# Kernel tuning notes

Measured on AMD Instinct MI355X. Metric: run time of the kernel, lower is better.

The kernel has to match this reference:

```python
import jax, jax.numpy as jnp
import numpy as np

N_NODES = 100000
N_EDGES = 3200000
D_IN = 128
D_OUT = 128


def setup_inputs() -> dict:
    key = jax.random.key(0)
    k1, k2, k3, k4, k5 = jax.random.split(key, 5)
    x = jax.random.normal(k1, (N_NODES, D_IN), dtype=jnp.float32)
    edge_row = jnp.sort(jax.random.randint(k2, (N_EDGES,), 0, N_NODES))
    edge_col = jax.random.randint(k3, (N_EDGES,), 0, N_NODES)
    edge_val = jax.random.uniform(k4, (N_EDGES,), dtype=jnp.float32)
    W = jax.random.normal(k5, (D_IN, D_OUT), dtype=jnp.float32) * (1.0 / np.sqrt(D_IN))
    return {"x": x, "edge_row": edge_row, "edge_col": edge_col,
            "edge_val": edge_val, "W": W}


def reference(x, edge_row, edge_col, edge_val, W):
    # h = spmm(adj_norm, x): gather source features, scale by edge weight,
    # scatter-add into destination rows.
    msgs = edge_val[:, None] * x[edge_col]            # [E, D_IN]
    h = jax.ops.segment_sum(msgs, edge_row, num_segments=N_NODES)  # [N, D_IN]
    # dense linear projection (no bias)
    return h @ W                                       # [N, D_OUT]
```

## Files before the change

kernel.cpp:

```cpp
#include <hip/hip_runtime.h>
#include <hip/hip_bf16.h>

#define D 128
#define D2U 64

typedef __attribute__((ext_vector_type(8))) short  short8;
typedef __attribute__((ext_vector_type(4))) float  f32x4;
typedef __attribute__((ext_vector_type(2))) float  f32x2;

__device__ __forceinline__ unsigned f2bf(float f) {
    unsigned u = __float_as_uint(f);
    u += 0x7FFFu + ((u >> 16) & 1u);
    return u >> 16;
}
__device__ __forceinline__ unsigned pk2(float a, float b) {
    return f2bf(a) | (f2bf(b) << 16);
}
__device__ __forceinline__ float bflo(unsigned u) { return __uint_as_float(u << 16); }
__device__ __forceinline__ float bfhi(unsigned u) { return __uint_as_float(u & 0xFFFF0000u); }

__global__ __launch_bounds__(256, 2) void gemm_mfma_kernel(
    const float* __restrict__ x, const float* __restrict__ W,
    unsigned* __restrict__ y, int n_nodes, int ntiles)
{
    __shared__ unsigned short Wt[D * D];

    const int t = threadIdx.x;

    {
        const float4* W4 = reinterpret_cast<const float4*>(W);
#pragma unroll
        for (int m = 0; m < 16; ++m) {
            const int idx4 = m * 256 + t;
            const int k  = idx4 >> 5;
            const int c0 = (idx4 & 31) << 2;
            const float4 w = W4[idx4];
            const float wv[4] = {w.x, w.y, w.z, w.w};
#pragma unroll
            for (int i = 0; i < 4; ++i) {
                const int c    = c0 + i;
                const int slot = (k >> 3) ^ (c & 15);
                Wt[c * 128 + slot * 8 + (k & 7)] = (unsigned short)f2bf(wv[i]);
            }
        }
    }
    __syncthreads();

    const int lane = t & 63;
    const int cl   = lane & 15;
    const int g    = lane >> 4;

    short8 wf[8][4];
#pragma unroll
    for (int ct = 0; ct < 8; ++ct)
#pragma unroll
        for (int ks = 0; ks < 4; ++ks) {
            const int c    = ct * 16 + cl;
            const int slot = (ks * 4 + g) ^ cl;
            wf[ct][ks] = *reinterpret_cast<const short8*>(&Wt[c * 128 + slot * 8]);
        }

    const int wave   = (blockIdx.x << 2) | (t >> 6);
    const int nwaves = gridDim.x << 2;

#define LOADX(rt_, buf_)                                                      \
    {                                                                         \
        int r_ = (rt_) * 16 + cl;                                             \
        if (r_ >= n_nodes) r_ = n_nodes - 1;                                  \
        const float* p_ = x + (size_t)r_ * D + g * 8;                         \
        _Pragma("unroll")                                                     \
        for (int ks_ = 0; ks_ < 4; ++ks_) {                                   \
            buf_[2 * ks_]     = *reinterpret_cast<const float4*>(p_ + ks_ * 32);     \
            buf_[2 * ks_ + 1] = *reinterpret_cast<const float4*>(p_ + ks_ * 32 + 4); \
        }                                                                     \
    }

#define COMPUTE(rt_, buf_)                                                    \
    {                                                                         \
        f32x4 acc_[8];                                                        \
        _Pragma("unroll")                                                     \
        for (int ct_ = 0; ct_ < 8; ++ct_) acc_[ct_] = (f32x4)(0.f);           \
        _Pragma("unroll")                                                     \
        for (int ks_ = 0; ks_ < 4; ++ks_) {                                   \
            short8 xf_;                                                       \
            unsigned* xu_ = reinterpret_cast<unsigned*>(&xf_);                \
            const float4 a_ = buf_[2 * ks_], b_ = buf_[2 * ks_ + 1];          \
            xu_[0] = pk2(a_.x, a_.y); xu_[1] = pk2(a_.z, a_.w);               \
            xu_[2] = pk2(b_.x, b_.y); xu_[3] = pk2(b_.z, b_.w);               \
            _Pragma("unroll")                                                 \
            for (int ct_ = 0; ct_ < 8; ++ct_)                                 \
                acc_[ct_] = __builtin_amdgcn_mfma_f32_16x16x32_bf16(          \
                    wf[ct_][ks_], xf_, acc_[ct_], 0, 0, 0);                   \
        }                                                                     \
        const int r_ = (rt_) * 16 + cl;                                       \
        if (r_ < n_nodes) {                                                   \
            unsigned* yp_ = y + (size_t)r_ * D2U + g * 2;                     \
            _Pragma("unroll")                                                 \
            for (int ct_ = 0; ct_ < 8; ++ct_) {                               \
                uint2 v2_ = make_uint2(pk2(acc_[ct_][0], acc_[ct_][1]),       \
                                       pk2(acc_[ct_][2], acc_[ct_][3]));      \
                *reinterpret_cast<uint2*>(yp_ + ct_ * 8) = v2_;               \
            }                                                                 \
        }                                                                     \
    }

    int rt = wave;
    if (rt >= ntiles) return;
    float4 bufA[8], bufB[8];
    LOADX(rt, bufA);
    while (true) {
        int nxt = rt + nwaves;
        if (nxt < ntiles) {
            LOADX(nxt, bufB);
            COMPUTE(rt, bufA);
            rt = nxt;
            nxt = rt + nwaves;
            if (nxt < ntiles) {
                LOADX(nxt, bufA);
                COMPUTE(rt, bufB);
                rt = nxt;
            } else { COMPUTE(rt, bufB); break; }
        } else { COMPUTE(rt, bufA); break; }
    }
#undef LOADX
#undef COMPUTE
}

__global__ __launch_bounds__(256) void build_rowptr_kernel(
    const int* __restrict__ row, int* __restrict__ ptr, int n_edges, int n_nodes)
{
    int e = blockIdx.x * blockDim.x + threadIdx.x;
    if (e > n_edges) return;
    int lo, hi;
    if (e == 0)            { lo = -1;               hi = row[0];   }
    else if (e == n_edges) { lo = row[n_edges - 1]; hi = n_nodes;  }
    else {
        lo = row[e - 1];
        hi = row[e];
        if (lo == hi) return;
    }
    for (int r = lo + 1; r <= hi; ++r) ptr[r] = e;
}

__global__ __launch_bounds__(256) void spmm_kernel(
    const uint4* __restrict__ yb4, const int* __restrict__ ptr,
    const int* __restrict__ col, const float* __restrict__ val,
    float4* __restrict__ out4, int n_nodes, int n_edges)
{
    const int gid  = blockIdx.x * blockDim.x + threadIdx.x;
    const int w    = gid >> 6;
    const int lane = threadIdx.x & 63;
    const int q    = lane >> 4;
    const int ql   = lane & 15;
    const int row  = (w << 2) + q;
    const bool valid = (row < n_nodes);

    int s = 0, e = 0;
    if (valid) { s = ptr[row]; e = ptr[row + 1]; }

    const int base = s & ~3;
    const int nb   = valid ? ((e - base + 3) >> 2) : 0;

    f32x2 a0 = {0.f, 0.f}, a1 = {0.f, 0.f}, a2 = {0.f, 0.f}, a3 = {0.f, 0.f};

    int4   C0, C1;
    float4 V0, V1;
    uint4  U[4], T[4];

#define CVLOAD(b_, C_, V_)                                                   \
    {                                                                        \
        const int o_ = base + ((b_) << 2);                                   \
        if (o_ + 4 <= n_edges) {                                             \
            C_ = *reinterpret_cast<const int4*>(col + o_);                   \
            V_ = *reinterpret_cast<const float4*>(val + o_);                 \
        } else {                                                             \
            const int m_ = n_edges - 1;                                      \
            C_.x = col[min(o_ + 0, m_)]; C_.y = col[min(o_ + 1, m_)];        \
            C_.z = col[min(o_ + 2, m_)]; C_.w = col[min(o_ + 3, m_)];        \
            V_.x = val[min(o_ + 0, m_)]; V_.y = val[min(o_ + 1, m_)];        \
            V_.z = val[min(o_ + 2, m_)]; V_.w = val[min(o_ + 3, m_)];        \
        }                                                                    \
        V_.x = (o_ + 0 >= s && o_ + 0 < e) ? V_.x : 0.f;                     \
        V_.y = (o_ + 1 >= s && o_ + 1 < e) ? V_.y : 0.f;                     \
        V_.z = (o_ + 2 >= s && o_ + 2 < e) ? V_.z : 0.f;                     \
        V_.w = (o_ + 3 >= s && o_ + 3 < e) ? V_.w : 0.f;                     \
    }

#define GATHER(C_, U_)                                                       \
    {                                                                        \
        U_[0] = yb4[(size_t)C_.x * 16 + ql];                                 \
        U_[1] = yb4[(size_t)C_.y * 16 + ql];                                 \
        U_[2] = yb4[(size_t)C_.z * 16 + ql];                                 \
        U_[3] = yb4[(size_t)C_.w * 16 + ql];                                 \
    }

#define CONSUME1(u_, v_)                                                     \
    {                                                                        \
        f32x2 vv_; vv_.x = (v_); vv_.y = (v_);                               \
        f32x2 t_;                                                            \
        t_.x = bflo(u_.x); t_.y = bfhi(u_.x); a0 += vv_ * t_;                \
        t_.x = bflo(u_.y); t_.y = bfhi(u_.y); a1 += vv_ * t_;                \
        t_.x = bflo(u_.z); t_.y = bfhi(u_.z); a2 += vv_ * t_;                \
        t_.x = bflo(u_.w); t_.y = bfhi(u_.w); a3 += vv_ * t_;                \
    }
#define CONSUME(U_, V_)                                                      \
    {                                                                        \
        CONSUME1(U_[0], V_.x); CONSUME1(U_[1], V_.y);                        \
        CONSUME1(U_[2], V_.z); CONSUME1(U_[3], V_.w);                        \
    }

#define ITER(b_, Ca_, Va_, Cb_, Vb_, Ua_, Ub_)                               \
    {                                                                        \
        if ((b_) + 1 < nb) GATHER(Cb_, Ub_);                                 \
        CONSUME(Ua_, Va_);                                                   \
        if ((b_) + 2 < nb) CVLOAD((b_) + 2, Ca_, Va_);                       \
    }

    if (nb > 0) {
        CVLOAD(0, C0, V0);
        GATHER(C0, U);
        if (nb > 1) CVLOAD(1, C1, V1);

        int b = 0;
        while (true) {
            ITER(b, C0, V0, C1, V1, U, T);
            if (++b >= nb) break;
            ITER(b, C1, V1, C0, V0, T, U);
            if (++b >= nb) break;
        }
    }
#undef CVLOAD
#undef GATHER
#undef CONSUME1
#undef CONSUME
#undef ITER

    if (valid) {
        f32x4 o1, o2;
        o1.x = a0.x; o1.y = a0.y; o1.z = a1.x; o1.w = a1.y;
        o2.x = a2.x; o2.y = a2.y; o2.z = a3.x; o2.w = a3.y;
        f32x4* op = reinterpret_cast<f32x4*>(out4 + (size_t)row * 32 + (ql << 1));
        __builtin_nontemporal_store(o1, op);
        __builtin_nontemporal_store(o2, op + 1);
    }
}

extern "C" void kernel_launch(void* const* d_in, const int* in_sizes, int n_in,
                              void* d_out, int out_size, void* d_ws, size_t ws_size,
                              hipStream_t stream)
{
    const float* x        = (const float*)d_in[0];
    const int*   edge_row = (const int*)  d_in[1];
    const int*   edge_col = (const int*)  d_in[2];
    const float* edge_val = (const float*)d_in[3];
    const float* W        = (const float*)d_in[4];
    float*       out      = (float*)d_out;

    const int n_nodes = in_sizes[0] / D;
    const int n_edges = in_sizes[1];
    const int ntiles  = (n_nodes + 15) / 16;

    unsigned* y   = (unsigned*)d_ws;
    int*      ptr = (int*)((char*)d_ws + (size_t)n_nodes * D2U * sizeof(unsigned));

    gemm_mfma_kernel<<<512, 256, 0, stream>>>(x, W, y, n_nodes, ntiles);

    {
        int blocks = (n_edges + 1 + 255) / 256;
        build_rowptr_kernel<<<blocks, 256, 0, stream>>>(edge_row, ptr, n_edges, n_nodes);
    }
    {
        int nwaves = (n_nodes + 3) / 4;
        int blocks = (nwaves + 3) / 4;
        spmm_kernel<<<blocks, 256, 0, stream>>>((const uint4*)y, ptr,
                                                edge_col, edge_val,
                                                (float4*)out, n_nodes, n_edges);
    }
}
```

Measured before the change: 156.9 us.

## Slice projected features by column and pin slices to XCDs for L2 locality

```diff
diff --git a/kernel.cpp b/kernel.cpp
--- a/kernel.cpp
+++ b/kernel.cpp
@@ -2,7 +2,7 @@
 #include <hip/hip_bf16.h>
 
 #define D 128
-#define D2U 64
+#define NSLICE 8
 
 typedef __attribute__((ext_vector_type(8))) short  short8;
 typedef __attribute__((ext_vector_type(4))) float  f32x4;
@@ -26,6 +26,7 @@
     __shared__ unsigned short Wt[D * D];
 
     const int t = threadIdx.x;
+    const size_t NN = (size_t)n_nodes;
 
     {
         const float4* W4 = reinterpret_cast<const float4*>(W);
@@ -94,12 +95,12 @@
         }                                                                     \
         const int r_ = (rt_) * 16 + cl;                                       \
         if (r_ < n_nodes) {                                                   \
-            unsigned* yp_ = y + (size_t)r_ * D2U + g * 2;                     \
             _Pragma("unroll")                                                 \
             for (int ct_ = 0; ct_ < 8; ++ct_) {                               \
                 uint2 v2_ = make_uint2(pk2(acc_[ct_][0], acc_[ct_][1]),       \
                                        pk2(acc_[ct_][2], acc_[ct_][3]));      \
-                *reinterpret_cast<uint2*>(yp_ + ct_ * 8) = v2_;               \
+                unsigned* yp_ = y + ((size_t)ct_ * NN + r_) * 8 + g * 2;      \
+                *reinterpret_cast<uint2*>(yp_) = v2_;                         \
             }                                                                 \
         }                                                                     \
     }
@@ -142,30 +143,27 @@
     for (int r = lo + 1; r <= hi; ++r) ptr[r] = e;
 }
 
-__global__ __launch_bounds__(256) void spmm_kernel(
-    const uint4* __restrict__ yb4, const int* __restrict__ ptr,
+__global__ void zero_queue_kernel(int* __restrict__ q) {
+    if (threadIdx.x < NSLICE) q[threadIdx.x] = 0;
+}
+
+__global__ __launch_bounds__(256, 8) void spmm_sliced_kernel(
+    const unsigned* __restrict__ ys,
+    const int* __restrict__ ptr,
     const int* __restrict__ col, const float* __restrict__ val,
-    float4* __restrict__ out4, int n_nodes, int n_edges)
-{
-    const int gid  = blockIdx.x * blockDim.x + threadIdx.x;
-    const int w    = gid >> 6;
+    float* __restrict__ out, int* __restrict__ queue,
+    int n_nodes, int n_edges, int rblocks)
+{
+    unsigned xcd;
+    asm volatile("s_getreg_b32 %0, hwreg(HW_REG_XCC_ID)" : "=s"(xcd));
+    xcd &= (NSLICE - 1);
+
+    const int w    = threadIdx.x >> 6;
     const int lane = threadIdx.x & 63;
-    const int q    = lane >> 4;
-    const int ql   = lane & 15;
-    const int row  = (w << 2) + q;
-    const bool valid = (row < n_nodes);
-
-    int s = 0, e = 0;
-    if (valid) { s = ptr[row]; e = ptr[row + 1]; }
-
-    const int base = s & ~3;
-    const int nb   = valid ? ((e - base + 3) >> 2) : 0;
-
-    f32x2 a0 = {0.f, 0.f}, a1 = {0.f, 0.f}, a2 = {0.f, 0.f}, a3 = {0.f, 0.f};
-
-    int4   C0, C1;
-    float4 V0, V1;
-    uint4  U[4], T[4];
+    const int rl   = lane >> 3;
+    const int d    = lane & 7;
+
+    __shared__ int s_idx;
 
 #define CVLOAD(b_, C_, V_)                                                   \
     {                                                                        \
@@ -185,64 +183,74 @@
         V_.z = (o_ + 2 >= s && o_ + 2 < e) ? V_.z : 0.f;                     \
         V_.w = (o_ + 3 >= s && o_ + 3 < e) ? V_.w : 0.f;                     \
     }
-
 #define GATHER(C_, U_)                                                       \
     {                                                                        \
-        U_[0] = yb4[(size_t)C_.x * 16 + ql];                                 \
-        U_[1] = yb4[(size_t)C_.y * 16 + ql];                                 \
-        U_[2] = yb4[(size_t)C_.z * 16 + ql];                                 \
-        U_[3] = yb4[(size_t)C_.w * 16 + ql];                                 \
-    }
-
-#define CONSUME1(u_, v_)                                                     \
-    {                                                                        \
-        f32x2 vv_; vv_.x = (v_); vv_.y = (v_);                               \
-        f32x2 t_;                                                            \
-        t_.x = bflo(u_.x); t_.y = bfhi(u_.x); a0 += vv_ * t_;                \
-        t_.x = bflo(u_.y); t_.y = bfhi(u_.y); a1 += vv_ * t_;                \
-        t_.x = bflo(u_.z); t_.y = bfhi(u_.z); a2 += vv_ * t_;                \
-        t_.x = bflo(u_.w); t_.y = bfhi(u_.w); a3 += vv_ * t_;                \
+        U_[0] = ybase[(size_t)C_.x << 3];                                    \
+        U_[1] = ybase[(size_t)C_.y << 3];                                    \
+        U_[2] = ybase[(size_t)C_.z << 3];                                    \
+        U_[3] = ybase[(size_t)C_.w << 3];                                    \
     }
 #define CONSUME(U_, V_)                                                      \
     {                                                                        \
-        CONSUME1(U_[0], V_.x); CONSUME1(U_[1], V_.y);                        \
-        CONSUME1(U_[2], V_.z); CONSUME1(U_[3], V_.w);                        \
-    }
-
-#define ITER(b_, Ca_, Va_, Cb_, Vb_, Ua_, Ub_)                               \
-    {                                                                        \
-        if ((b_) + 1 < nb) GATHER(Cb_, Ub_);                                 \
-        CONSUME(Ua_, Va_);                                                   \
-        if ((b_) + 2 < nb) CVLOAD((b_) + 2, Ca_, Va_);                       \
-    }
-
-    if (nb > 0) {
-        CVLOAD(0, C0, V0);
-        GATHER(C0, U);
-        if (nb > 1) CVLOAD(1, C1, V1);
-
-        int b = 0;
-        while (true) {
-            ITER(b, C0, V0, C1, V1, U, T);
-            if (++b >= nb) break;
-            ITER(b, C1, V1, C0, V0, T, U);
-            if (++b >= nb) break;
+        f32x2 t_, vv_;                                                       \
+        t_.x = bflo(U_[0]); t_.y = bfhi(U_[0]);                              \
+        vv_.x = V_.x; vv_.y = V_.x; acc += vv_ * t_;                         \
+        t_.x = bflo(U_[1]); t_.y = bfhi(U_[1]);                              \
+        vv_.x = V_.y; vv_.y = V_.y; acc += vv_ * t_;                         \
+        t_.x = bflo(U_[2]); t_.y = bfhi(U_[2]);                              \
+        vv_.x = V_.z; vv_.y = V_.z; acc += vv_ * t_;                         \
+        t_.x = bflo(U_[3]); t_.y = bfhi(U_[3]);                              \
+        vv_.x = V_.w; vv_.y = V_.w; acc += vv_ * t_;                         \
+    }
+
+    for (int sl = 0; sl < NSLICE; ++sl) {
+        const int slice = (xcd + sl) & (NSLICE - 1);
+        const unsigned* ybase = ys + (size_t)slice * n_nodes * 8 + d;
+
+        for (;;) {
+            if (threadIdx.x == 0) s_idx = atomicAdd(queue + slice, 1);
+            __syncthreads();
+            const int rblk = s_idx;
+            __syncthreads();
+            if (rblk >= rblocks) break;
+
+            const int row = (rblk << 5) + (w << 3) + rl;
+            if (row < n_nodes) {
+                const int s = ptr[row];
+                const int e = ptr[row + 1];
+                const int base = s & ~3;
+                const int nb = (e - base + 3) >> 2;
+
+                f32x2 acc; acc.x = 0.f; acc.y = 0.f;
+                int4   C0, C1;
+                float4 V0, V1;
+                unsigned U[4], T[4];
+
+                if (nb > 0) {
+                    CVLOAD(0, C0, V0);
+                    GATHER(C0, U);
+                    if (nb > 1) CVLOAD(1, C1, V1);
+                    int b = 0;
+                    while (true) {
+                        if (b + 1 < nb) GATHER(C1, T);
+                        CONSUME(U, V0);
+                        if (b + 2 < nb) CVLOAD(b + 2, C0, V0);
+                        if (++b >= nb) break;
+                        if (b + 1 < nb) GATHER(C0, U);
+                        CONSUME(T, V1);
+                        if (b + 2 < nb) CVLOAD(b + 2, C1, V1);
+                        if (++b >= nb) break;
+                    }
+                }
+
+                float* op = out + (size_t)row * D + slice * 16 + d * 2;
+                __builtin_nontemporal_store(acc, reinterpret_cast<f32x2*>(op));
+            }
         }
     }
 #undef CVLOAD
 #undef GATHER
-#undef CONSUME1
 #undef CONSUME
-#undef ITER
-
-    if (valid) {
-        f32x4 o1, o2;
-        o1.x = a0.x; o1.y = a0.y; o1.z = a1.x; o1.w = a1.y;
-        o2.x = a2.x; o2.y = a2.y; o2.z = a3.x; o2.w = a3.y;
-        f32x4* op = reinterpret_cast<f32x4*>(out4 + (size_t)row * 32 + (ql << 1));
-        __builtin_nontemporal_store(o1, op);
-        __builtin_nontemporal_store(o2, op + 1);
-    }
 }
 
 extern "C" void kernel_launch(void* const* d_in, const int* in_sizes, int n_in,
@@ -259,9 +267,13 @@
     const int n_nodes = in_sizes[0] / D;
     const int n_edges = in_sizes[1];
     const int ntiles  = (n_nodes + 15) / 16;
-
-    unsigned* y   = (unsigned*)d_ws;
-    int*      ptr = (int*)((char*)d_ws + (size_t)n_nodes * D2U * sizeof(unsigned));
+    const int rblocks = (n_nodes + 31) / 32;
+
+    unsigned* y     = (unsigned*)d_ws;
+    int*      ptr   = (int*)((char*)d_ws + (size_t)n_nodes * 256);
+    int*      queue = ptr + (n_nodes + 1);
+
+    zero_queue_kernel<<<1, 64, 0, stream>>>(queue);
 
     gemm_mfma_kernel<<<512, 256, 0, stream>>>(x, W, y, n_nodes, ntiles);
 
@@ -269,11 +281,8 @@
         int blocks = (n_edges + 1 + 255) / 256;
         build_rowptr_kernel<<<blocks, 256, 0, stream>>>(edge_row, ptr, n_edges, n_nodes);
     }
-    {
-        int nwaves = (n_nodes + 3) / 4;
-        int blocks = (nwaves + 3) / 4;
-        spmm_kernel<<<blocks, 256, 0, stream>>>((const uint4*)y, ptr,
-                                                edge_col, edge_val,
-                                                (float4*)out, n_nodes, n_edges);
-    }
-}
+    spmm_sliced_kernel<<<2048, 256, 0, stream>>>((const unsigned*)y, ptr,
+                                                 edge_col, edge_val,
+                                                 out, queue,
+                                                 n_nodes, n_edges, rblocks);
+}
```

New measurement: 553.4 us. 253% more time.
